# Kernel optimization log

Hardware: AMD Instinct MI355X
Metric: run time of the kernel (lower is better)

Reference implementation:

```python
import jax, jax.numpy as jnp
import numpy as np

N_CLASSES = 5
IGNORE = 255
IMAX = 32  # max instance index value (indexes in [1, IMAX])


def setup_inputs() -> dict:
    key = jax.random.key(0)
    k1, k2, k3 = jax.random.split(key, 3)
    B, D, H, W = 8, 128, 512, 512
    feature_out = jax.random.normal(k1, (B, D, H, W), dtype=jnp.float32)
    labels = jax.random.randint(k2, (B, H, W), 0, N_CLASSES).astype(jnp.int32)
    indexes = jax.random.randint(k3, (B, H, W), 1, IMAX + 1).astype(jnp.int32)
    return {"feature_out": feature_out, "labels": labels, "indexes": indexes}


def _lintra(feature_out, labels, indexes):
    # Semantics of the torch module (sort + boundary detection + python loops),
    # re-expressed as a fused segment reduction:
    #  - per-image segments are (label, instance-index) pairs among non-ignore pixels
    #  - segments with key==0 (ignore) or with a single pixel are excluded
    #  - per (image, class): instance means F [K, D], ret = mean_{i,j,d} |F_i - F_j|
    #    (includes i==j diagonal, as in the original KxK broadcast), then smooth-L1
    #  - final loss = mean over all (image, class) losses / B
    B, D, H, W = feature_out.shape
    feats = jnp.transpose(feature_out, (0, 2, 3, 1)).reshape(B * H * W, D)
    lab = labels.reshape(B, -1)
    idx = indexes.reshape(B, -1)
    valid = lab != IGNORE
    lab = jnp.where(valid, lab, 0)
    idx = jnp.where(valid, idx, 0)
    S = N_CLASSES * (IMAX + 1)
    seg = lab * (IMAX + 1) + idx                      # 0 marks ignore pixels
    gseg = (seg + jnp.arange(B, dtype=seg.dtype)[:, None] * S).reshape(-1)
    sums = jax.ops.segment_sum(feats, gseg, num_segments=B * S)
    counts = jax.ops.segment_sum(jnp.ones((B * H * W,), feats.dtype), gseg,
                                 num_segments=B * S)
    means = sums / jnp.maximum(counts, 1.0)[:, None]
    means = means.reshape(B, N_CLASSES, IMAX + 1, D)
    counts = counts.reshape(B, N_CLASSES, IMAX + 1)
    inc = counts >= 2.0                               # singleton segments skipped
    inc = inc.at[:, :, 0].set(False)                  # key==0 slot (ignore) skipped
    incf = inc.astype(means.dtype)                    # [B, C, I]
    # intra-class pairwise |F_i - F_j|, masked to included instances
    diff = jnp.abs(means[:, :, :, None, :] - means[:, :, None, :, :])  # [B,C,I,I,D]
    pair = incf[:, :, :, None] * incf[:, :, None, :]                   # [B,C,I,I]
    ssum = jnp.einsum('bcijd,bcij->bc', diff, pair)
    K = incf.sum(-1)                                   # instances per (image,class)
    ret = jnp.where(K > 0, ssum / jnp.maximum(K * K * D, 1.0), 0.0)
    loss_bc = jnp.where(ret < 1.0, 0.5 * ret * ret, ret - 0.5)
    has = (K > 0).astype(ret.dtype)
    n = has.sum()
    total = jnp.where(n > 0, (loss_bc * has).sum() / jnp.maximum(n, 1.0), 0.0)
    return (total / B).reshape(1)


def reference(feature_out, labels, indexes):
    return _lintra(feature_out, labels, indexes)
```

## Files before the change

kernel.cpp:

```cpp
#include <hip/hip_runtime.h>
#include <stdint.h>

#define NC 5
#define IMAXP1 33
#define SEGS 165
#define SEGS_PAD 192
#define MT 6
#define HW_ (512 * 512)
#define IGNORE_L 255
#define KCHUNK 4096
#define NSUP (KCHUNK / 64)
#define TILE (SEGS_PAD * 128)

typedef __attribute__((ext_vector_type(8))) short short8v;
typedef __attribute__((ext_vector_type(16))) float f32x16;
typedef __attribute__((ext_vector_type(2))) unsigned short u16x2;
typedef __attribute__((ext_vector_type(2))) float float2v;
typedef __attribute__((ext_vector_type(2))) __bf16 bf16x2;
typedef __attribute__((ext_vector_type(2))) unsigned long long u64x2;

__global__ __launch_bounds__(256) void seg_count_kernel(
    const int* __restrict__ labels, const int* __restrict__ indexes,
    uint8_t* __restrict__ seg, unsigned* __restrict__ counts,
    int pix_per_block) {
  __shared__ unsigned hist[SEGS];
  for (int i = threadIdx.x; i < SEGS; i += blockDim.x) hist[i] = 0u;
  __syncthreads();

  const long long base = (long long)blockIdx.x * pix_per_block;
  const int b = (int)(base / HW_);
  const int nvec = pix_per_block / 4;
  const int4* lab4 = (const int4*)(labels + base);
  const int4* idx4 = (const int4*)(indexes + base);
  uchar4* seg4 = (uchar4*)(seg + base);

  for (int k = threadIdx.x; k < nvec; k += blockDim.x) {
    int4 l = lab4[k];
    int4 ix = idx4[k];
    int s0 = (l.x == IGNORE_L) ? 0 : l.x * IMAXP1 + ix.x;
    int s1 = (l.y == IGNORE_L) ? 0 : l.y * IMAXP1 + ix.y;
    int s2 = (l.z == IGNORE_L) ? 0 : l.z * IMAXP1 + ix.z;
    int s3 = (l.w == IGNORE_L) ? 0 : l.w * IMAXP1 + ix.w;
    uchar4 sv;
    sv.x = (unsigned char)s0; sv.y = (unsigned char)s1;
    sv.z = (unsigned char)s2; sv.w = (unsigned char)s3;
    seg4[k] = sv;
    atomicAdd(&hist[s0], 1u);
    atomicAdd(&hist[s1], 1u);
    atomicAdd(&hist[s2], 1u);
    atomicAdd(&hist[s3], 1u);
  }
  __syncthreads();
  for (int i = threadIdx.x; i < SEGS; i += blockDim.x)
    if (hist[i]) atomicAdd(&counts[b * SEGS + i], hist[i]);
}

struct SS {
  float4 f[8];
  u64x2 g0, g1;
};

__global__ __launch_bounds__(256, 2) void segsum_mfma_kernel(
    const float* __restrict__ feat, const uint8_t* __restrict__ seg,
    float* __restrict__ partials, int chunks_per_img) {
  __shared__ unsigned long long sseg8[KCHUNK / 8];
  const int b = blockIdx.x / chunks_per_img;
  const int chunk = blockIdx.x % chunks_per_img;
  const int pbase = chunk * KCHUNK;

  const unsigned long long* gseg8 =
      (const unsigned long long*)(seg + (size_t)b * HW_ + pbase);
  for (int i = threadIdx.x; i < KCHUNK / 8; i += 256) sseg8[i] = gseg8[i];
  __syncthreads();

  const int l = threadIdx.x & 63;
  const int w = threadIdx.x >> 6;
  const int lane31 = l & 31;
  const int hi = l >> 5;
  const int ch = w * 32 + lane31;

  const float4* fp4 =
      (const float4*)(feat + ((size_t)b * 128 + ch) * HW_ + pbase) + hi * 8;
  const uint8_t* sp = (const uint8_t*)sseg8 + hi * 32;

  const unsigned lane2 = (unsigned)lane31 | ((unsigned)lane31 << 16);

  f32x16 acc[MT];
  #pragma unroll
  for (int m = 0; m < MT; ++m) acc[m] = (f32x16)(0.f);

  #define LOAD_SS(dst, s)                                             \
    do {                                                              \
      _Pragma("unroll") for (int i = 0; i < 8; ++i)                   \
          (dst).f[i] = fp4[(size_t)(s)*16 + i];                       \
      const u64x2* sp2 = (const u64x2*)(sp + (s)*64);                 \
      (dst).g0 = sp2[0];                                              \
      (dst).g1 = sp2[1];                                              \
    } while (0)

  #define KSTEP(f0, f1, sb)                                           \
    do {                                                              \
      unsigned svp[4];                                                \
      _Pragma("unroll") for (int j = 0; j < 4; ++j) {                 \
        unsigned lo8 = (unsigned)(((sb) >> (16 * j)) & 0xFFull);      \
        unsigned hi8 = (unsigned)(((sb) >> (16 * j + 8)) & 0xFFull);  \
        svp[j] = (lo8 | (hi8 << 16)) ^ lane2;                         \
      }                                                               \
      float fs[8] = {(f0).x, (f0).y, (f0).z, (f0).w,                  \
                     (f1).x, (f1).y, (f1).z, (f1).w};                 \
      union { unsigned u[4]; short8v v; } bhi, blo;                   \
      _Pragma("unroll") for (int j = 0; j < 4; ++j) {                 \
        float2v f2 = {fs[2 * j], fs[2 * j + 1]};                      \
        bf16x2 h2 = __builtin_convertvector(f2, bf16x2);              \
        unsigned hb = __builtin_bit_cast(unsigned, h2);               \
        bhi.u[j] = hb;                                                \
        float fh0 = __builtin_bit_cast(float, hb << 16);              \
        float fh1 = __builtin_bit_cast(float, hb & 0xFFFF0000u);      \
        float2v l2 = {f2.x - fh0, f2.y - fh1};                        \
        bf16x2 lo2 = __builtin_convertvector(l2, bf16x2);             \
        blo.u[j] = __builtin_bit_cast(unsigned, lo2);                 \
      }                                                               \
      _Pragma("unroll") for (int m = 0; m < MT; ++m) {                \
        unsigned m2 = (unsigned)(m * 32) | ((unsigned)(m * 32) << 16);\
        union { unsigned u[4]; short8v v; } a;                        \
        _Pragma("unroll") for (int j = 0; j < 4; ++j) {               \
          u16x2 y = __builtin_bit_cast(u16x2, svp[j] ^ m2);           \
          u16x2 nz = __builtin_elementwise_min(y, (u16x2)(unsigned short)1); \
          u16x2 msk = nz - (u16x2)(unsigned short)1;                  \
          u16x2 av = msk & (u16x2)(unsigned short)0x3F80;             \
          a.u[j] = __builtin_bit_cast(unsigned, av);                  \
        }                                                             \
        acc[m] = __builtin_amdgcn_mfma_f32_32x32x16_bf16(a.v, bhi.v,  \
                                                         acc[m], 0, 0, 0); \
        acc[m] = __builtin_amdgcn_mfma_f32_32x32x16_bf16(a.v, blo.v,  \
                                                         acc[m], 0, 0, 0); \
      }                                                               \
    } while (0)

  #define COMPUTE_SS(src)                                             \
    do {                                                              \
      KSTEP((src).f[0], (src).f[1], (src).g0.x);                      \
      KSTEP((src).f[2], (src).f[3], (src).g0.y);                      \
      KSTEP((src).f[4], (src).f[5], (src).g1.x);                      \
      KSTEP((src).f[6], (src).f[7], (src).g1.y);                      \
    } while (0)

  SS bufA, bufB;
  LOAD_SS(bufA, 0);
  for (int s = 0; s < NSUP; s += 2) {
    LOAD_SS(bufB, s + 1);
    COMPUTE_SS(bufA);
    if (s + 2 < NSUP) LOAD_SS(bufA, s + 2);
    COMPUTE_SS(bufB);
  }

  float* pb = partials + (size_t)blockIdx.x * TILE;
  #pragma unroll
  for (int m = 0; m < MT; ++m) {
    #pragma unroll
    for (int r = 0; r < 16; ++r) {
      int s = m * 32 + (r & 3) + 8 * (r >> 2) + 4 * hi;
      pb[s * 128 + ch] = acc[m][r];
    }
  }
}

__global__ __launch_bounds__(256) void reduce_partials_kernel(
    const float* __restrict__ partials, float* __restrict__ sums,
    int chunks_per_img) {
  const int o = blockIdx.x * 256 + threadIdx.x;
  const int b = blockIdx.y;
  const float* p = partials + (size_t)b * chunks_per_img * TILE + o;
  float t = 0.f;
  for (int c = 0; c < chunks_per_img; ++c) t += p[(size_t)c * TILE];
  sums[(size_t)b * TILE + o] = t;
}

__global__ __launch_bounds__(256) void pairloss_kernel(
    const float* __restrict__ sums, const unsigned* __restrict__ counts,
    float* __restrict__ loss_sum, unsigned* __restrict__ nvalid, int D) {
  const int b = blockIdx.x / NC;
  const int c = blockIdx.x % NC;

  __shared__ float sh_mean[32 * 128];
  __shared__ float sh_cnt[IMAXP1];
  __shared__ int list[IMAXP1];
  __shared__ int Ksh;
  __shared__ uchar2 pairs[32 * 31 / 2];
  __shared__ double wred[4];

  if (threadIdx.x == 0) {
    int K = 0;
    for (int i = 1; i < IMAXP1; ++i) {
      unsigned cnt = counts[b * SEGS + c * IMAXP1 + i];
      if (cnt >= 2u) {
        list[K] = i;
        sh_cnt[K] = (float)cnt;
        ++K;
      }
    }
    Ksh = K;
    int p = 0;
    for (int i = 0; i < K; ++i)
      for (int j = i + 1; j < K; ++j) {
        pairs[p].x = (unsigned char)i;
        pairs[p].y = (unsigned char)j;
        ++p;
      }
  }
  __syncthreads();
  const int K = Ksh;
  if (K == 0) return;

  for (int idx = threadIdx.x; idx < K * D; idx += blockDim.x) {
    int k = idx / 128, d = idx % 128;
    int s = c * IMAXP1 + list[k];
    sh_mean[k * 128 + d] =
        sums[(size_t)b * TILE + s * 128 + d] / sh_cnt[k];
  }
  __syncthreads();

  const int npairs = K * (K - 1) / 2;
  const int total = npairs * 128;
  float local = 0.f;
  for (int idx = threadIdx.x; idx < total; idx += blockDim.x) {
    int p = idx >> 7, d = idx & 127;
    int i = pairs[p].x, j = pairs[p].y;
    local += fabsf(sh_mean[i * 128 + d] - sh_mean[j * 128 + d]);
  }

  double v = (double)local;
  #pragma unroll
  for (int off = 32; off; off >>= 1) v += __shfl_down(v, off, 64);
  const int wave = threadIdx.x >> 6;
  if ((threadIdx.x & 63) == 0) wred[wave] = v;
  __syncthreads();
  if (threadIdx.x == 0) {
    double ssum = 2.0 * (wred[0] + wred[1] + wred[2] + wred[3]);
    double ret = ssum / ((double)K * (double)K * (double)D);
    double loss = (ret < 1.0) ? 0.5 * ret * ret : ret - 0.5;
    atomicAdd(loss_sum, (float)loss);
    atomicAdd(nvalid, 1u);
  }
}

__global__ void finalize_kernel(const float* __restrict__ loss_sum,
                                const unsigned* __restrict__ nvalid,
                                float* __restrict__ out, int B) {
  if (threadIdx.x == 0) {
    unsigned n = *nvalid;
    out[0] = n ? (*loss_sum / (float)n) / (float)B : 0.f;
  }
}

extern "C" void kernel_launch(void* const* d_in, const int* in_sizes, int n_in,
                              void* d_out, int out_size, void* d_ws,
                              size_t ws_size, hipStream_t stream) {
  const float* feat = (const float*)d_in[0];
  const int* labels = (const int*)d_in[1];
  const int* indexes = (const int*)d_in[2];

  const int npix_total = in_sizes[1];
  const int B = npix_total / HW_;
  const int D = in_sizes[0] / npix_total;
  const int cpi = HW_ / KCHUNK;
  const int nblocks = B * cpi;

  uint8_t* seg = (uint8_t*)d_ws;
  size_t off = ((size_t)npix_total + 255) & ~(size_t)255;
  float* partials = (float*)((char*)d_ws + off);
  size_t part_bytes = (size_t)nblocks * TILE * sizeof(float);
  float* sums = (float*)((char*)d_ws + off + part_bytes);
  size_t sums_bytes = (size_t)B * TILE * sizeof(float);
  unsigned* counts = (unsigned*)((char*)d_ws + off + part_bytes + sums_bytes);
  size_t counts_bytes = (size_t)B * SEGS * sizeof(unsigned);
  float* loss_sum =
      (float*)((char*)d_ws + off + part_bytes + sums_bytes + counts_bytes);
  unsigned* nvalid = (unsigned*)(loss_sum + 1);

  hipMemsetAsync(counts, 0, counts_bytes + 2 * sizeof(unsigned), stream);

  const int pix_per_block = 4096;
  seg_count_kernel<<<npix_total / pix_per_block, 256, 0, stream>>>(
      labels, indexes, seg, counts, pix_per_block);

  segsum_mfma_kernel<<<nblocks, 256, 0, stream>>>(feat, seg, partials, cpi);

  dim3 rgrid(TILE / 256, B);
  reduce_partials_kernel<<<rgrid, 256, 0, stream>>>(partials, sums, cpi);

  pairloss_kernel<<<B * NC, 256, 0, stream>>>(sums, counts, loss_sum, nvalid,
                                              D);
  finalize_kernel<<<1, 64, 0, stream>>>(loss_sum, nvalid, (float*)d_out, B);
}
```

Before: 347.1 us.

## Stage feature tiles through LDS with coalesced row loads and split pixels across waves

The segment-sum MFMA kernel now gives each block 32 channels and a 16K-pixel chunk, staging 256-pixel slabs of 32 channel rows into double-buffered LDS with fully coalesced float4 loads. Each wave then reads its own 64-pixel slice from LDS, so every wave accumulates into its own partial tile instead of the old scheme where each lane streamed its channel row directly from global memory. The aim is better global-load coalescing and memory-level parallelism on the bandwidth-bound feature read, at the cost of LDS traffic, a barrier per stage and a larger partials buffer that the reduce kernel now has to sum over 64 slices.

```diff
diff --git a/kernel.cpp b/kernel.cpp
--- a/kernel.cpp
+++ b/kernel.cpp
@@ -8,16 +8,20 @@
 #define MT 6
 #define HW_ (512 * 512)
 #define IGNORE_L 255
-#define KCHUNK 4096
-#define NSUP (KCHUNK / 64)
 #define TILE (SEGS_PAD * 128)
+
+#define CHUNK_PX 16384
+#define STAGE_PX 256
+#define NSTAGE (CHUNK_PX / STAGE_PX)
+#define ROW_STRIDE 1040
+#define BUFSZ (32 * ROW_STRIDE)
+#define WTILE (SEGS_PAD * 32)
 
 typedef __attribute__((ext_vector_type(8))) short short8v;
 typedef __attribute__((ext_vector_type(16))) float f32x16;
 typedef __attribute__((ext_vector_type(2))) unsigned short u16x2;
 typedef __attribute__((ext_vector_type(2))) float float2v;
 typedef __attribute__((ext_vector_type(2))) __bf16 bf16x2;
-typedef __attribute__((ext_vector_type(2))) unsigned long long u64x2;
 
 __global__ __launch_bounds__(256) void seg_count_kernel(
     const int* __restrict__ labels, const int* __restrict__ indexes,
@@ -55,48 +59,33 @@
     if (hist[i]) atomicAdd(&counts[b * SEGS + i], hist[i]);
 }
 
-struct SS {
-  float4 f[8];
-  u64x2 g0, g1;
-};
-
 __global__ __launch_bounds__(256, 2) void segsum_mfma_kernel(
     const float* __restrict__ feat, const uint8_t* __restrict__ seg,
-    float* __restrict__ partials, int chunks_per_img) {
-  __shared__ unsigned long long sseg8[KCHUNK / 8];
-  const int b = blockIdx.x / chunks_per_img;
-  const int chunk = blockIdx.x % chunks_per_img;
-  const int pbase = chunk * KCHUNK;
-
-  const unsigned long long* gseg8 =
-      (const unsigned long long*)(seg + (size_t)b * HW_ + pbase);
-  for (int i = threadIdx.x; i < KCHUNK / 8; i += 256) sseg8[i] = gseg8[i];
-  __syncthreads();
+    float* __restrict__ partials) {
+  __shared__ __align__(16) char sbuf[2 * BUFSZ];
+
+  const int bid = blockIdx.x;
+  const int b = bid >> 6;
+  const int g = (bid >> 4) & 3;
+  const int chunk = bid & 15;
+  const int P0 = chunk * CHUNK_PX;
 
   const int l = threadIdx.x & 63;
   const int w = threadIdx.x >> 6;
   const int lane31 = l & 31;
   const int hi = l >> 5;
-  const int ch = w * 32 + lane31;
-
-  const float4* fp4 =
-      (const float4*)(feat + ((size_t)b * 128 + ch) * HW_ + pbase) + hi * 8;
-  const uint8_t* sp = (const uint8_t*)sseg8 + hi * 32;
 
   const unsigned lane2 = (unsigned)lane31 | ((unsigned)lane31 << 16);
+
+  const float* gbase =
+      feat + ((size_t)(b * 128 + g * 32 + w * 8)) * HW_ + P0 + l * 4;
+  char* lwbase = sbuf + (w * 8) * ROW_STRIDE + l * 16;
+  const char* lrbase = sbuf + lane31 * ROW_STRIDE;
+  const uint8_t* segg = seg + (size_t)b * HW_ + P0 + w * 64 + hi * 8;
 
   f32x16 acc[MT];
   #pragma unroll
   for (int m = 0; m < MT; ++m) acc[m] = (f32x16)(0.f);
-
-  #define LOAD_SS(dst, s)                                             \
-    do {                                                              \
-      _Pragma("unroll") for (int i = 0; i < 8; ++i)                   \
-          (dst).f[i] = fp4[(size_t)(s)*16 + i];                       \
-      const u64x2* sp2 = (const u64x2*)(sp + (s)*64);                 \
-      (dst).g0 = sp2[0];                                              \
-      (dst).g1 = sp2[1];                                              \
-    } while (0)
 
   #define KSTEP(f0, f1, sb)                                           \
     do {                                                              \
@@ -137,42 +126,63 @@
       }                                                               \
     } while (0)
 
-  #define COMPUTE_SS(src)                                             \
-    do {                                                              \
-      KSTEP((src).f[0], (src).f[1], (src).g0.x);                      \
-      KSTEP((src).f[2], (src).f[3], (src).g0.y);                      \
-      KSTEP((src).f[4], (src).f[5], (src).g1.x);                      \
-      KSTEP((src).f[6], (src).f[7], (src).g1.y);                      \
-    } while (0)
-
-  SS bufA, bufB;
-  LOAD_SS(bufA, 0);
-  for (int s = 0; s < NSUP; s += 2) {
-    LOAD_SS(bufB, s + 1);
-    COMPUTE_SS(bufA);
-    if (s + 2 < NSUP) LOAD_SS(bufA, s + 2);
-    COMPUTE_SS(bufB);
-  }
-
-  float* pb = partials + (size_t)blockIdx.x * TILE;
+  {
+    float4 st[8];
+    #pragma unroll
+    for (int j = 0; j < 8; ++j) st[j] = *(const float4*)(gbase + (size_t)j * HW_);
+    #pragma unroll
+    for (int j = 0; j < 8; ++j) *(float4*)(lwbase + j * ROW_STRIDE) = st[j];
+  }
+  __syncthreads();
+
+  for (int s = 0; s < NSTAGE; ++s) {
+    const int buf = s & 1;
+    float4 nx[8];
+    if (s + 1 < NSTAGE) {
+      #pragma unroll
+      for (int j = 0; j < 8; ++j)
+        nx[j] = *(const float4*)(gbase + (size_t)j * HW_ + (s + 1) * STAGE_PX);
+    }
+
+    const char* lb = lrbase + buf * BUFSZ;
+    const uint8_t* sgs = segg + s * STAGE_PX;
+    #pragma unroll
+    for (int t = 0; t < 4; ++t) {
+      const int kb = w * 64 + t * 16;
+      float4 v0 = *(const float4*)(lb + (kb + hi * 8) * 4);
+      float4 v1 = *(const float4*)(lb + (kb + hi * 8) * 4 + 16);
+      unsigned long long sb = *(const unsigned long long*)(sgs + t * 16);
+      KSTEP(v0, v1, sb);
+    }
+
+    if (s + 1 < NSTAGE) {
+      #pragma unroll
+      for (int j = 0; j < 8; ++j)
+        *(float4*)(lwbase + (buf ^ 1) * BUFSZ + j * ROW_STRIDE) = nx[j];
+    }
+    __syncthreads();
+  }
+
+  float* pb = partials + ((size_t)bid * 4 + w) * WTILE;
   #pragma unroll
   for (int m = 0; m < MT; ++m) {
     #pragma unroll
     for (int r = 0; r < 16; ++r) {
-      int s = m * 32 + (r & 3) + 8 * (r >> 2) + 4 * hi;
-      pb[s * 128 + ch] = acc[m][r];
+      int srow = m * 32 + (r & 3) + 8 * (r >> 2) + 4 * hi;
+      pb[srow * 32 + lane31] = acc[m][r];
     }
   }
 }
 
 __global__ __launch_bounds__(256) void reduce_partials_kernel(
-    const float* __restrict__ partials, float* __restrict__ sums,
-    int chunks_per_img) {
+    const float* __restrict__ partials, float* __restrict__ sums) {
   const int o = blockIdx.x * 256 + threadIdx.x;
   const int b = blockIdx.y;
-  const float* p = partials + (size_t)b * chunks_per_img * TILE + o;
+  const int s = o >> 7, ch = o & 127, g = ch >> 5, n = ch & 31;
+  const float* p = partials + (size_t)(b * 4 + g) * 64 * WTILE + s * 32 + n;
   float t = 0.f;
-  for (int c = 0; c < chunks_per_img; ++c) t += p[(size_t)c * TILE];
+  #pragma unroll 4
+  for (int u = 0; u < 64; ++u) t += p[(size_t)u * WTILE];
   sums[(size_t)b * TILE + o] = t;
 }
 
@@ -263,13 +273,12 @@
   const int npix_total = in_sizes[1];
   const int B = npix_total / HW_;
   const int D = in_sizes[0] / npix_total;
-  const int cpi = HW_ / KCHUNK;
-  const int nblocks = B * cpi;
+  const int nblocks = B * 4 * (HW_ / CHUNK_PX);
 
   uint8_t* seg = (uint8_t*)d_ws;
   size_t off = ((size_t)npix_total + 255) & ~(size_t)255;
   float* partials = (float*)((char*)d_ws + off);
-  size_t part_bytes = (size_t)nblocks * TILE * sizeof(float);
+  size_t part_bytes = (size_t)nblocks * 4 * WTILE * sizeof(float);
   float* sums = (float*)((char*)d_ws + off + part_bytes);
   size_t sums_bytes = (size_t)B * TILE * sizeof(float);
   unsigned* counts = (unsigned*)((char*)d_ws + off + part_bytes + sums_bytes);
@@ -284,10 +293,10 @@
   seg_count_kernel<<<npix_total / pix_per_block, 256, 0, stream>>>(
       labels, indexes, seg, counts, pix_per_block);
 
-  segsum_mfma_kernel<<<nblocks, 256, 0, stream>>>(feat, seg, partials, cpi);
+  segsum_mfma_kernel<<<nblocks, 256, 0, stream>>>(feat, seg, partials);
 
   dim3 rgrid(TILE / 256, B);
-  reduce_partials_kernel<<<rgrid, 256, 0, stream>>>(partials, sums, cpi);
+  reduce_partials_kernel<<<rgrid, 256, 0, stream>>>(partials, sums);
 
   pairloss_kernel<<<B * NC, 256, 0, stream>>>(sums, counts, loss_sum, nvalid,
                                               D);
```

New measurement: 556.7 us. 60.4% more time.
